# Kernel optimization log

Hardware: AMD Instinct MI355X
Metric: run time of the kernel (lower is better)

Reference implementation:

```python
import jax, jax.numpy as jnp
import numpy as np

EPS = 1e-8  # torch cosine_similarity denominator clamp


def setup_inputs() -> dict:
    key = jax.random.key(0)
    k1, k2, k3 = jax.random.split(key, 3)
    x = jax.random.normal(k1, (4, 512, 256, 256), dtype=jnp.float32)
    v0 = jax.random.normal(k2, (4, 256, 14, 14), dtype=jnp.float32)
    v1 = jax.random.normal(k3, (4, 256, 14, 14), dtype=jnp.float32)
    return {"x": x, "v0": v0, "v1": v1}


def reference(x, v0, v1):
    # CoLoc_Sel.AV_default_forward with C=2, att_type='cos'
    C = 2
    B, D, F, T = x.shape
    Dc = D // C
    H, W = v0.shape[2], v0.shape[3]

    # AdaptiveMaxPool3d((None,1,1)) on (B,D,F,T): global max over (F,T)
    xp = jnp.max(x, axis=(2, 3)).reshape(B, C, Dc)          # (B,C,Dc) = split blocks
    # x_p1 = blocks in order, x_p2 = reversed; stacked -> permutations P=2
    x_t = jnp.stack([xp, xp[:, ::-1]], axis=1)              # (B,P,C,Dc)

    v_cat = jnp.stack([v0, v1], axis=1)                     # (B,C,Dc,H,W)

    # cosine similarity along the Dc axis, broadcast over P and (H,W)
    dot = jnp.einsum('bpcd,bcdhw->bpchw', x_t, v_cat)       # (B,P,C,H,W)
    xn = jnp.sqrt(jnp.sum(x_t * x_t, axis=3))               # (B,P,C)
    vn = jnp.sqrt(jnp.sum(v_cat * v_cat, axis=2))           # (B,C,H,W)
    maps = dot / jnp.maximum(xn[..., None, None] * vn[:, None], EPS)  # (B,P,C,H,W)

    # per-permutation score: max over (H,W), sum over C
    scores = jnp.sum(jnp.max(maps, axis=(3, 4)), axis=-1)   # (B,P)
    order = jnp.argsort(-scores, axis=1)                    # descending
    ss = jnp.take_along_axis(scores, order, axis=1)
    match_loss = jnp.mean(-ss[:, 0] + jnp.sum(ss[:, 1:], axis=-1))

    maps_sorted = jnp.take_along_axis(maps, order[:, :, None, None, None], axis=1)
    att_maps = maps_sorted[:, 0]                            # (B,C,H,W)

    # pick visual feature vector at argmax spatial location of each att map
    max_ind = jnp.argmax(att_maps.reshape(B, C, H * W), axis=-1)        # (B,C)
    v_flat = v_cat.reshape(B, C, Dc, H * W)
    v_sel = jnp.take_along_axis(v_flat, max_ind[:, :, None, None], axis=3)  # (B,C,Dc,1)

    feats = [jnp.broadcast_to(v_sel[:, c, :, :, None], (B, Dc, F, T)) for c in range(C)]
    out = jnp.concatenate([*feats, x], axis=1)              # (B, 2*D, F, T)
    return out, match_loss, att_maps
```

## Files before the change

kernel.cpp:

```cpp
#include <hip/hip_runtime.h>
#include <hip/hip_bf16.h>
#include <float.h>
#include <math.h>

constexpr int B  = 4;
constexpr int D  = 512;
constexpr int C  = 2;
constexpr int Dc = 256;
constexpr int FT = 256 * 256;
constexpr int HW = 14 * 14;
constexpr int OUTC = 2 * Dc + D;
constexpr float EPSV = 1e-8f;

typedef float f4 __attribute__((ext_vector_type(4)));


__global__ __launch_bounds__(256) void kA_maxcopy(const float* __restrict__ x,
                                                  float* __restrict__ out,
                                                  float* __restrict__ xp) {
    const int slice = blockIdx.x;
    const int b = slice / D;
    const int d = slice % D;
    const f4* xs = (const f4*)(x + (size_t)slice * FT);
    f4* os = (f4*)(out + ((size_t)(b * OUTC + 2 * Dc + d)) * FT);
    float m = -FLT_MAX;
    for (int i0 = threadIdx.x; i0 < FT / 4; i0 += 256 * 8) {
        f4 v[8];
        #pragma unroll
        for (int u = 0; u < 8; ++u)
            v[u] = __builtin_nontemporal_load(&xs[i0 + u * 256]);
        #pragma unroll
        for (int u = 0; u < 8; ++u) {
            os[i0 + u * 256] = v[u];
            m = fmaxf(m, fmaxf(fmaxf(v[u].x, v[u].y), fmaxf(v[u].z, v[u].w)));
        }
    }
    for (int off = 32; off; off >>= 1) m = fmaxf(m, __shfl_down(m, off, 64));
    __shared__ float sm[4];
    if ((threadIdx.x & 63) == 0) sm[threadIdx.x >> 6] = m;
    __syncthreads();
    if (threadIdx.x == 0) {
        xp[slice] = fmaxf(fmaxf(sm[0], sm[1]), fmaxf(sm[2], sm[3]));
    }
}

__global__ __launch_bounds__(256) void kB_maps(const float* __restrict__ v0,
                                               const float* __restrict__ v1,
                                               const float* __restrict__ xp,
                                               float* __restrict__ maps,
                                               float* __restrict__ mx,
                                               int* __restrict__ amax) {
    const int bc = blockIdx.x;
    const int b = bc / C, c = bc % C;
    const int tid = threadIdx.x;

    __shared__ float sxc[Dc], sxo[Dc];
    sxc[tid] = xp[(b * C + c) * Dc + tid];
    sxo[tid] = xp[(b * C + (1 - c)) * Dc + tid];
    __syncthreads();

    float ec = sxc[tid] * sxc[tid];
    float eo = sxo[tid] * sxo[tid];
    for (int off = 32; off; off >>= 1) {
        ec += __shfl_down(ec, off, 64);
        eo += __shfl_down(eo, off, 64);
    }
    __shared__ float red[8];
    const int lane = tid & 63, wid = tid >> 6;
    if (lane == 0) { red[wid] = ec; red[4 + wid] = eo; }
    __syncthreads();
    __shared__ float s_xn_c, s_xn_o;
    if (tid == 0) {
        s_xn_c = sqrtf(red[0] + red[1] + red[2] + red[3]);
        s_xn_o = sqrtf(red[4] + red[5] + red[6] + red[7]);
    }
    __syncthreads();
    const float xn_c = s_xn_c, xn_o = s_xn_o;

    float map0 = -FLT_MAX, map1 = -FLT_MAX;
    if (tid < HW) {
        const float* vv = (c == 0 ? v0 : v1) + (size_t)b * Dc * HW;
        float d0 = 0.f, d1 = 0.f, vs = 0.f;
        for (int dc = 0; dc < Dc; ++dc) {
            float v = vv[dc * HW + tid];
            d0 = fmaf(sxc[dc], v, d0);
            d1 = fmaf(sxo[dc], v, d1);
            vs = fmaf(v, v, vs);
        }
        float vn = sqrtf(vs);
        map0 = d0 / fmaxf(xn_c * vn, EPSV);
        map1 = d1 / fmaxf(xn_o * vn, EPSV);
        maps[((b * 2 + 0) * C + c) * HW + tid] = map0;
        maps[((b * 2 + 1) * C + c) * HW + tid] = map1;
    }

    __shared__ float rv[256];
    __shared__ int ri[256];
    for (int p = 0; p < 2; ++p) {
        __syncthreads();
        rv[tid] = (tid < HW) ? (p == 0 ? map0 : map1) : -FLT_MAX;
        ri[tid] = tid;
        __syncthreads();
        for (int s = 128; s; s >>= 1) {
            if (tid < s) {
                float v2 = rv[tid + s]; int i2 = ri[tid + s];
                if (v2 > rv[tid] || (v2 == rv[tid] && i2 < ri[tid])) {
                    rv[tid] = v2; ri[tid] = i2;
                }
            }
            __syncthreads();
        }
        if (tid == 0) {
            mx[(b * 2 + p) * C + c] = rv[0];
            amax[(b * 2 + p) * C + c] = ri[0];
        }
    }
}

__global__ __launch_bounds__(256) void kC_select(const float* __restrict__ maps,
                                                 const float* __restrict__ mx,
                                                 const int* __restrict__ amax,
                                                 float* __restrict__ out,
                                                 int* __restrict__ mind) {
    __shared__ int pbest[B];
    const int tid = threadIdx.x;
    if (tid == 0) {
        float L = 0.f;
        for (int b = 0; b < B; ++b) {
            float s0 = mx[(b * 2 + 0) * C + 0] + mx[(b * 2 + 0) * C + 1];
            float s1 = mx[(b * 2 + 1) * C + 0] + mx[(b * 2 + 1) * C + 1];
            int p = (s1 > s0) ? 1 : 0;
            pbest[b] = p;
            L += p ? (s0 - s1) : (s1 - s0);
        }
        out[(size_t)B * OUTC * FT] = L / (float)B;
    }
    __syncthreads();
    const size_t att_off = (size_t)B * OUTC * FT + 1;
    for (int i = tid; i < B * C * HW; i += blockDim.x) {
        int b = i / (C * HW);
        int r = i % (C * HW);
        int c = r / HW;
        int hw = r % HW;
        out[att_off + i] = maps[((b * 2 + pbest[b]) * C + c) * HW + hw];
    }
    if (tid < B * C) {
        int b = tid / C, c = tid % C;
        mind[tid] = amax[(b * 2 + pbest[b]) * C + c];
    }
}

__global__ __launch_bounds__(256) void kD_fill(const float* __restrict__ v0,
                                               const float* __restrict__ v1,
                                               const int* __restrict__ mind,
                                               float* __restrict__ out) {
    const int n = blockIdx.x;
    const int b = n / (2 * Dc);
    const int r = n % (2 * Dc);
    const int c = r / Dc;
    const int dc = r % Dc;
    const int hw = mind[b * C + c];
    const float* vv = (c == 0 ? v0 : v1);
    const float val = vv[((size_t)(b * Dc + dc)) * HW + hw];
    f4 v4 = {val, val, val, val};
    f4* os = (f4*)(out + ((size_t)(b * OUTC + c * Dc + dc)) * FT);
    for (int i0 = threadIdx.x; i0 < FT / 4; i0 += 256 * 8) {
        #pragma unroll
        for (int u = 0; u < 8; ++u)
            os[i0 + u * 256] = v4;
    }
}

extern "C" void kernel_launch(void* const* d_in, const int* in_sizes, int n_in,
                              void* d_out, int out_size, void* d_ws, size_t ws_size,
                              hipStream_t stream) {
    const float* x  = (const float*)d_in[0];
    const float* v0 = (const float*)d_in[1];
    const float* v1 = (const float*)d_in[2];
    float* out = (float*)d_out;
    float* ws = (float*)d_ws;

    float* xp   = ws;
    float* maps = ws + 2048;
    float* mx   = ws + 5184;
    int*   amax = (int*)(ws + 5200);
    int*   mind = (int*)(ws + 5216);

    kA_maxcopy<<<B * D, 256, 0, stream>>>(x, out, xp);
    kB_maps<<<B * C, 256, 0, stream>>>(v0, v1, xp, maps, mx, amax);
    kC_select<<<1, 256, 0, stream>>>(maps, mx, amax, out, mind);
    kD_fill<<<B * 2 * Dc, 256, 0, stream>>>(v0, v1, mind, out);
}
```

Baseline: 317.8 us.

## Fold map/select tail into last block of max-copy kernel, use nontemporal stores

Merges the small cosine-map and selection kernels into the max-copy kernel: the last block to finish, detected with an atomic counter, computes norms, maps, argmaxes, loss and att-map output in shared memory. This removes two kernel launches and their global round trips. Stores of the big copy and fill are also switched to nontemporal. The tail now runs on a single block, with less parallelism than the previous 8-block maps kernel, and an extra memset is added per call.

```diff
diff --git a/kernel.cpp b/kernel.cpp
--- a/kernel.cpp
+++ b/kernel.cpp
@@ -15,138 +15,138 @@
 typedef float f4 __attribute__((ext_vector_type(4)));
 
 
-__global__ __launch_bounds__(256) void kA_maxcopy(const float* __restrict__ x,
-                                                  float* __restrict__ out,
-                                                  float* __restrict__ xp) {
+__global__ __launch_bounds__(256) void kA_maxcopy_fold(const float* __restrict__ x,
+                                                       const float* __restrict__ v0,
+                                                       const float* __restrict__ v1,
+                                                       float* __restrict__ out,
+                                                       float* __restrict__ xp,
+                                                       int* __restrict__ mind,
+                                                       int* __restrict__ counter) {
+    const int tid = threadIdx.x;
     const int slice = blockIdx.x;
     const int b = slice / D;
     const int d = slice % D;
     const f4* xs = (const f4*)(x + (size_t)slice * FT);
     f4* os = (f4*)(out + ((size_t)(b * OUTC + 2 * Dc + d)) * FT);
     float m = -FLT_MAX;
-    for (int i0 = threadIdx.x; i0 < FT / 4; i0 += 256 * 8) {
+    for (int i0 = tid; i0 < FT / 4; i0 += 256 * 8) {
         f4 v[8];
         #pragma unroll
         for (int u = 0; u < 8; ++u)
             v[u] = __builtin_nontemporal_load(&xs[i0 + u * 256]);
         #pragma unroll
         for (int u = 0; u < 8; ++u) {
-            os[i0 + u * 256] = v[u];
+            __builtin_nontemporal_store(v[u], &os[i0 + u * 256]);
             m = fmaxf(m, fmaxf(fmaxf(v[u].x, v[u].y), fmaxf(v[u].z, v[u].w)));
         }
     }
     for (int off = 32; off; off >>= 1) m = fmaxf(m, __shfl_down(m, off, 64));
     __shared__ float sm[4];
-    if ((threadIdx.x & 63) == 0) sm[threadIdx.x >> 6] = m;
+    if ((tid & 63) == 0) sm[tid >> 6] = m;
     __syncthreads();
-    if (threadIdx.x == 0) {
+    __shared__ int s_last;
+    if (tid == 0) {
         xp[slice] = fmaxf(fmaxf(sm[0], sm[1]), fmaxf(sm[2], sm[3]));
+        __threadfence();
+        int t = atomicAdd(counter, 1);
+        s_last = (t == gridDim.x - 1) ? 1 : 0;
     }
-}
+    __syncthreads();
+    if (!s_last) return;
 
-__global__ __launch_bounds__(256) void kB_maps(const float* __restrict__ v0,
-                                               const float* __restrict__ v1,
-                                               const float* __restrict__ xp,
-                                               float* __restrict__ maps,
-                                               float* __restrict__ mx,
-                                               int* __restrict__ amax) {
-    const int bc = blockIdx.x;
-    const int b = bc / C, c = bc % C;
-    const int tid = threadIdx.x;
+    __threadfence();
 
-    __shared__ float sxc[Dc], sxo[Dc];
-    sxc[tid] = xp[(b * C + c) * Dc + tid];
-    sxo[tid] = xp[(b * C + (1 - c)) * Dc + tid];
+    __shared__ float sxp[2048];
+    __shared__ float smaps[16 * HW];
+    __shared__ float s_xn[8];
+    __shared__ float s_mx[16];
+    __shared__ int   s_ai[16];
+    __shared__ int   s_pb[B];
+    __shared__ float cand_v[256];
+    __shared__ int   cand_i[256];
+
+    #pragma unroll
+    for (int k = 0; k < 8; ++k) sxp[tid + k * 256] = xp[tid + k * 256];
     __syncthreads();
 
-    float ec = sxc[tid] * sxc[tid];
-    float eo = sxo[tid] * sxo[tid];
-    for (int off = 32; off; off >>= 1) {
-        ec += __shfl_down(ec, off, 64);
-        eo += __shfl_down(eo, off, 64);
-    }
-    __shared__ float red[8];
-    const int lane = tid & 63, wid = tid >> 6;
-    if (lane == 0) { red[wid] = ec; red[4 + wid] = eo; }
-    __syncthreads();
-    __shared__ float s_xn_c, s_xn_o;
-    if (tid == 0) {
-        s_xn_c = sqrtf(red[0] + red[1] + red[2] + red[3]);
-        s_xn_o = sqrtf(red[4] + red[5] + red[6] + red[7]);
+    {
+        const int g = tid >> 5, l = tid & 31;
+        float acc = 0.f;
+        for (int dc = l; dc < Dc; dc += 32) {
+            float v = sxp[g * Dc + dc];
+            acc = fmaf(v, v, acc);
+        }
+        for (int off = 16; off; off >>= 1) acc += __shfl_down(acc, off, 32);
+        if (l == 0) s_xn[g] = sqrtf(acc);
     }
     __syncthreads();
-    const float xn_c = s_xn_c, xn_o = s_xn_o;
 
-    float map0 = -FLT_MAX, map1 = -FLT_MAX;
-    if (tid < HW) {
-        const float* vv = (c == 0 ? v0 : v1) + (size_t)b * Dc * HW;
-        float d0 = 0.f, d1 = 0.f, vs = 0.f;
-        for (int dc = 0; dc < Dc; ++dc) {
-            float v = vv[dc * HW + tid];
-            d0 = fmaf(sxc[dc], v, d0);
-            d1 = fmaf(sxo[dc], v, d1);
-            vs = fmaf(v, v, vs);
-        }
-        float vn = sqrtf(vs);
-        map0 = d0 / fmaxf(xn_c * vn, EPSV);
-        map1 = d1 / fmaxf(xn_o * vn, EPSV);
-        maps[((b * 2 + 0) * C + c) * HW + tid] = map0;
-        maps[((b * 2 + 1) * C + c) * HW + tid] = map1;
-    }
-
-    __shared__ float rv[256];
-    __shared__ int ri[256];
-    for (int p = 0; p < 2; ++p) {
-        __syncthreads();
-        rv[tid] = (tid < HW) ? (p == 0 ? map0 : map1) : -FLT_MAX;
-        ri[tid] = tid;
-        __syncthreads();
-        for (int s = 128; s; s >>= 1) {
-            if (tid < s) {
-                float v2 = rv[tid + s]; int i2 = ri[tid + s];
-                if (v2 > rv[tid] || (v2 == rv[tid] && i2 < ri[tid])) {
-                    rv[tid] = v2; ri[tid] = i2;
-                }
+    {
+        const int g = tid >> 5, l = tid & 31;
+        const int bb = g >> 1, c = g & 1;
+        const float* vv = (c == 0 ? v0 : v1) + (size_t)bb * Dc * HW;
+        const float* xc = sxp + (bb * C + c) * Dc;
+        const float* xo = sxp + (bb * C + (1 - c)) * Dc;
+        const float xn_c = s_xn[bb * C + c];
+        const float xn_o = s_xn[bb * C + (1 - c)];
+        for (int hw = l; hw < HW; hw += 32) {
+            float d0 = 0.f, d1 = 0.f, vs = 0.f;
+            for (int dc = 0; dc < Dc; ++dc) {
+                float v = vv[dc * HW + hw];
+                d0 = fmaf(xc[dc], v, d0);
+                d1 = fmaf(xo[dc], v, d1);
+                vs = fmaf(v, v, vs);
             }
-            __syncthreads();
-        }
-        if (tid == 0) {
-            mx[(b * 2 + p) * C + c] = rv[0];
-            amax[(b * 2 + p) * C + c] = ri[0];
+            const float vn = sqrtf(vs);
+            smaps[(bb * 4 + 0 * 2 + c) * HW + hw] = d0 / fmaxf(xn_c * vn, EPSV);
+            smaps[(bb * 4 + 1 * 2 + c) * HW + hw] = d1 / fmaxf(xn_o * vn, EPSV);
         }
     }
-}
+    __syncthreads();
 
-__global__ __launch_bounds__(256) void kC_select(const float* __restrict__ maps,
-                                                 const float* __restrict__ mx,
-                                                 const int* __restrict__ amax,
-                                                 float* __restrict__ out,
-                                                 int* __restrict__ mind) {
-    __shared__ int pbest[B];
-    const int tid = threadIdx.x;
+    {
+        const int row = tid >> 4, sub = tid & 15;
+        float bv = -FLT_MAX; int bi = HW;
+        for (int hw = sub; hw < HW; hw += 16) {
+            float v = smaps[row * HW + hw];
+            if (v > bv) { bv = v; bi = hw; }
+        }
+        cand_v[tid] = bv; cand_i[tid] = bi;
+        __syncthreads();
+        if (sub == 0) {
+            float mv = -FLT_MAX; int mi = 0;
+            for (int k = 0; k < 16; ++k) {
+                float v = cand_v[row * 16 + k]; int idx = cand_i[row * 16 + k];
+                if (v > mv || (v == mv && idx < mi)) { mv = v; mi = idx; }
+            }
+            s_mx[row] = mv; s_ai[row] = mi;
+        }
+    }
+    __syncthreads();
+
     if (tid == 0) {
         float L = 0.f;
-        for (int b = 0; b < B; ++b) {
-            float s0 = mx[(b * 2 + 0) * C + 0] + mx[(b * 2 + 0) * C + 1];
-            float s1 = mx[(b * 2 + 1) * C + 0] + mx[(b * 2 + 1) * C + 1];
-            int p = (s1 > s0) ? 1 : 0;
-            pbest[b] = p;
+        for (int bb = 0; bb < B; ++bb) {
+            const float s0 = s_mx[bb * 4 + 0] + s_mx[bb * 4 + 1];
+            const float s1 = s_mx[bb * 4 + 2] + s_mx[bb * 4 + 3];
+            const int p = (s1 > s0) ? 1 : 0;
+            s_pb[bb] = p;
             L += p ? (s0 - s1) : (s1 - s0);
         }
         out[(size_t)B * OUTC * FT] = L / (float)B;
     }
     __syncthreads();
+
     const size_t att_off = (size_t)B * OUTC * FT + 1;
-    for (int i = tid; i < B * C * HW; i += blockDim.x) {
-        int b = i / (C * HW);
-        int r = i % (C * HW);
-        int c = r / HW;
-        int hw = r % HW;
-        out[att_off + i] = maps[((b * 2 + pbest[b]) * C + c) * HW + hw];
+    for (int i = tid; i < B * C * HW; i += 256) {
+        const int bb = i / (C * HW);
+        const int r = i % (C * HW);
+        const int c = r / HW, hw = r % HW;
+        out[att_off + i] = smaps[(bb * 4 + s_pb[bb] * 2 + c) * HW + hw];
     }
     if (tid < B * C) {
-        int b = tid / C, c = tid % C;
-        mind[tid] = amax[(b * 2 + pbest[b]) * C + c];
+        const int bb = tid / C, c = tid % C;
+        mind[tid] = s_ai[bb * 4 + s_pb[bb] * 2 + c];
     }
 }
 
@@ -167,7 +167,7 @@
     for (int i0 = threadIdx.x; i0 < FT / 4; i0 += 256 * 8) {
         #pragma unroll
         for (int u = 0; u < 8; ++u)
-            os[i0 + u * 256] = v4;
+            __builtin_nontemporal_store(v4, &os[i0 + u * 256]);
     }
 }
 
@@ -180,14 +180,12 @@
     float* out = (float*)d_out;
     float* ws = (float*)d_ws;
 
-    float* xp   = ws;
-    float* maps = ws + 2048;
-    float* mx   = ws + 5184;
-    int*   amax = (int*)(ws + 5200);
-    int*   mind = (int*)(ws + 5216);
+    float* xp      = ws;
+    int*   counter = (int*)(ws + 2048);
+    int*   mind    = (int*)(ws + 2052);
 
-    kA_maxcopy<<<B * D, 256, 0, stream>>>(x, out, xp);
-    kB_maps<<<B * C, 256, 0, stream>>>(v0, v1, xp, maps, mx, amax);
-    kC_select<<<1, 256, 0, stream>>>(maps, mx, amax, out, mind);
+    hipMemsetAsync(counter, 0, sizeof(int), stream);
+
+    kA_maxcopy_fold<<<B * D, 256, 0, stream>>>(x, v0, v1, out, xp, mind, counter);
     kD_fill<<<B * 2 * Dc, 256, 0, stream>>>(v0, v1, mind, out);
 }
```

New measurement: 461.0 us. 45.1% more time.
